# Kernel optimization log

Measured on AMD Instinct MI355X. Metric: run time of the kernel, lower is better.

The kernel has to match this reference:

```python
import jax, jax.numpy as jnp
import numpy as np

DT = 0.001
HIDDEN = 512
OUT = 128

def setup_inputs() -> dict:
    key = jax.random.key(0)
    k1, k2 = jax.random.split(key)
    x = jax.random.normal(k1, (64, 2048, HIDDEN), dtype=jnp.float32)
    # torch Linear default init ~ U(-1/sqrt(fan_in), 1/sqrt(fan_in)), weight shape [out, in]
    lim = 1.0 / np.sqrt(HIDDEN)
    W = jax.random.uniform(k2, (OUT, HIDDEN), dtype=jnp.float32, minval=-lim, maxval=lim)
    tau_syn = jnp.asarray(0.5, dtype=jnp.float32)  # tau_syn_out (used as tau_syn_inv)
    tau_mem = jnp.asarray(0.5, dtype=jnp.float32)  # tau_mem_out (used as tau_mem_inv)
    return {"x": x, "W": W, "tau_syn": tau_syn, "tau_mem": tau_mem}

def reference(x, W, tau_syn, tau_mem):
    # SNNDecode.forward: clamp taus, permute to [seq, batch, in], per-step
    # Linear + norse LI (leaky integrator) feed-forward step with v_leak = 0.
    tau_syn = jnp.clip(tau_syn, 0.0, 1.0)
    tau_mem = jnp.clip(tau_mem, 0.0, 1.0)
    batch, seq, _ = x.shape
    # The per-step Linear is recurrence-independent: hoist it into one big GEMM.
    # z_all: [seq, batch, out]
    z_all = jnp.einsum('bsh,oh->sbo', x, W)
    v0 = jnp.zeros((batch, OUT), dtype=x.dtype)
    i0 = jnp.zeros((batch, OUT), dtype=x.dtype)

    def step(carry, z):
        v, i = carry
        # li_feed_forward_step: dv = dt*tau_mem_inv*((v_leak - v) + i)
        v_new = v + DT * tau_mem * (i - v)
        i_dec = i - DT * tau_syn * i
        i_new = i_dec + z
        return (v_new, i_new), v_new

    (v_f, i_f), voltages = jax.lax.scan(step, (v0, i0), z_all)
    # output stacked over time: [seq, batch, out]; final state (v, i)
    return voltages, v_f, i_f
```

## Files before the change

### kernel.cpp

```cpp
#include <hip/hip_runtime.h>
#include <hip/hip_bf16.h>


typedef __attribute__((ext_vector_type(4))) float          f4;
typedef __attribute__((ext_vector_type(8))) short          s8;
typedef __attribute__((ext_vector_type(4))) unsigned       u4;
typedef __attribute__((ext_vector_type(2))) unsigned       u2;
typedef __attribute__((ext_vector_type(4))) unsigned short su4;

#define SEQ    2048
#define HID    512
#define CHAINS 8192
#define VOLT   16777216
#define NCH    64
#define CHUNK  32

__device__ __forceinline__ float clamp01(float x) { return fminf(fmaxf(x, 0.f), 1.f); }

__device__ __forceinline__ unsigned pkbf(float x, float y) {
  float2 t; t.x = x; t.y = y;
  union { __hip_bfloat162 h; unsigned u; } c;
  c.h = __float22bfloat162_rn(t);
  return c.u;
}

__device__ __forceinline__ unsigned short f2bf(float f) {
  union { float f; unsigned u; } c; c.f = f;
  unsigned u = c.u;
  unsigned r = (u + 0x7fffu + ((u >> 16) & 1u)) >> 16;
  return (unsigned short)r;
}

__device__ __forceinline__ float bf2f(unsigned short s) {
  union { unsigned u; float f; } c; c.u = ((unsigned)s) << 16; return c.f;
}

__device__ __forceinline__ int swz(int row, int k) {
  return (row * 64 + k) ^ ((row & 7) << 3);
}

__global__ __launch_bounds__(256) void k_wconv(const float* __restrict__ W,
                                               unsigned short* __restrict__ Wb) {
  const int i = blockIdx.x * 256 + threadIdx.x;
  const f4 lo = ((const f4*)W)[2 * i];
  const f4 hi = ((const f4*)W)[2 * i + 1];
  su4 v0, v1;
#pragma unroll
  for (int j = 0; j < 4; ++j) { v0[j] = f2bf(lo[j]); v1[j] = f2bf(hi[j]); }
  ((su4*)Wb)[2 * i] = v0;
  ((su4*)Wb)[2 * i + 1] = v1;
}

template <int ZB>
__global__ __launch_bounds__(256, 2) void k_gemm(const float* __restrict__ X,
                                                 const unsigned short* __restrict__ Wb,
                                                 float* __restrict__ Out,
                                                 unsigned short* __restrict__ zbf,
                                                 const float* __restrict__ tau_syn,
                                                 const float* __restrict__ tau_mem,
                                                 float* __restrict__ ws) {
  __shared__ __align__(16) char smem[65536];
  short* const AS = (short*)smem;
  float* const ZS = (float*)smem;

  const int tid = threadIdx.x;
  const int blk = blockIdx.x;
  const int m0  = blk << 7;
  const int bI  = blk >> 4;
  const int t0  = (blk & 15) << 7;

  const int rbase = tid >> 3;
  const int coff  = (tid & 7) << 3;

  const int lane = tid & 63;
  const int wid  = tid >> 6;
  const int wmb  = (wid >> 1) << 6;
  const int wnb  = (wid & 1) << 6;
  const int lr   = lane & 15;
  const int lk   = (lane >> 4) << 3;

  const float* pX[4];
#pragma unroll
  for (int c = 0; c < 4; ++c)
    pX[c] = X + (size_t)(m0 + (c << 5) + rbase) * HID + coff;
  const unsigned short* pB[4];
#pragma unroll
  for (int ni = 0; ni < 4; ++ni)
    pB[ni] = Wb + (size_t)(wnb + (ni << 4) + lr) * HID + lk;

  f4 acc[4][4];
#pragma unroll
  for (int mi = 0; mi < 4; ++mi)
#pragma unroll
    for (int ni = 0; ni < 4; ++ni) acc[mi][ni] = (f4){0.f, 0.f, 0.f, 0.f};

  f4 xa[3][4][2];
#pragma unroll
  for (int c = 0; c < 4; ++c) {
    xa[0][c][0] = *(const f4*)(pX[c]);
    xa[0][c][1] = *(const f4*)(pX[c] + 4);
    xa[1][c][0] = *(const f4*)(pX[c] + 64);
    xa[1][c][1] = *(const f4*)(pX[c] + 68);
  }

#pragma unroll
  for (int ks = 0; ks < 8; ++ks) {
    const int cur = ks % 3;
    short* const Ac = AS + ((ks & 1) << 13);
#pragma unroll
    for (int c = 0; c < 4; ++c) {
      const int row = (c << 5) + rbase;
      u4 va;
      va[0] = pkbf(xa[cur][c][0][0], xa[cur][c][0][1]);
      va[1] = pkbf(xa[cur][c][0][2], xa[cur][c][0][3]);
      va[2] = pkbf(xa[cur][c][1][0], xa[cur][c][1][1]);
      va[3] = pkbf(xa[cur][c][1][2], xa[cur][c][1][3]);
      *(u4*)&Ac[swz(row, coff)] = va;
    }
    __syncthreads();
    s8 bg[2][4];
#pragma unroll
    for (int kk = 0; kk < 2; ++kk)
#pragma unroll
      for (int ni = 0; ni < 4; ++ni)
        bg[kk][ni] = *(const s8*)(pB[ni] + (ks << 6) + (kk << 5));
    if (ks < 6) {
      const int k0 = (ks + 2) << 6;
      const int nxt = (ks + 2) % 3;
#pragma unroll
      for (int c = 0; c < 4; ++c) {
        xa[nxt][c][0] = *(const f4*)(pX[c] + k0);
        xa[nxt][c][1] = *(const f4*)(pX[c] + k0 + 4);
      }
    }
#pragma unroll
    for (int kk = 0; kk < 2; ++kk) {
      s8 af[4];
#pragma unroll
      for (int mi = 0; mi < 4; ++mi)
        af[mi] = *(const s8*)&Ac[swz(wmb + (mi << 4) + lr, (kk << 5) + lk)];
#pragma unroll
      for (int mi = 0; mi < 4; ++mi)
#pragma unroll
        for (int ni = 0; ni < 4; ++ni)
          acc[mi][ni] = __builtin_amdgcn_mfma_f32_16x16x32_bf16(af[mi], bg[kk][ni],
                                                                acc[mi][ni], 0, 0, 0);
    }
  }

  __syncthreads();
  const int rr = (lane >> 4) << 2;
#pragma unroll
  for (int mi = 0; mi < 4; ++mi)
#pragma unroll
    for (int ni = 0; ni < 4; ++ni)
#pragma unroll
      for (int r = 0; r < 4; ++r)
        ZS[(wmb + (mi << 4) + rr + r) * 128 + wnb + (ni << 4) + lr] = acc[mi][ni][r];
  __syncthreads();

  if (ZB) {
    unsigned short* const Zrow = zbf + (size_t)t0 * 8192 + (bI << 7);
#pragma unroll
    for (int i = 0; i < 16; ++i) {
      const int idx  = (i << 8) + tid;
      const int toff = idx >> 5;
      const int c4   = idx & 31;
      const f4 zv = *(const f4*)&ZS[toff * 128 + (c4 << 2)];
      u2 pk; pk[0] = pkbf(zv[0], zv[1]); pk[1] = pkbf(zv[2], zv[3]);
      *(u2*)(Zrow + (size_t)toff * 8192 + (c4 << 2)) = pk;
    }
  } else {
    float* const Zrow = Out + (size_t)t0 * 8192 + (bI << 7);
#pragma unroll
    for (int i = 0; i < 16; ++i) {
      const int idx  = (i << 8) + tid;
      const int toff = idx >> 5;
      const int c4   = idx & 31;
      *(f4*)(Zrow + (size_t)toff * 8192 + (c4 << 2)) = *(const f4*)&ZS[toff * 128 + (c4 << 2)];
    }
  }
  {
    const float a  = 0.001f * clamp01(tau_mem[0]);
    const float eb = 1.f - 0.001f * clamp01(tau_syn[0]);
    const int col = tid & 127, h = tid >> 7;
    const int chain = (bI << 7) + col;
#pragma unroll
    for (int s = 0; s < 2; ++s) {
      const int r0 = (h << 6) + (s << 5);
      const float* zs = ZS + r0 * 128 + col;
      float v = 0.f, ii = 0.f;
#pragma unroll 8
      for (int j = 0; j < CHUNK; ++j) {
        const float z = zs[j * 128];
        v  = v + a * (ii - v);
        ii = eb * ii + z;
      }
      const int q = ((blk & 15) << 2) + (h << 1) + s;
      ws[q * CHAINS + chain]                 = v;
      ws[NCH * CHAINS + q * CHAINS + chain]  = ii;
    }
  }
}

__global__ __launch_bounds__(256) void k_comb(const float* __restrict__ tau_syn,
                                              const float* __restrict__ tau_mem,
                                              float* __restrict__ Out,
                                              float* __restrict__ ws) {
  __shared__ __align__(16) f4 SV[NCH][4], SI[NCH][4];
  const int tid = threadIdx.x;
  const int q   = tid >> 2;
  const int s   = tid & 3;
  const int cg  = blockIdx.x * 4 + s;
  const float a  = 0.001f * clamp01(tau_mem[0]);
  const float bb = 0.001f * clamp01(tau_syn[0]);
  const float ea = 1.f - a, eb = 1.f - bb;
  float P = 1.f, Q = 0.f, R = 1.f;
#pragma unroll
  for (int j = 0; j < CHUNK; ++j) { const float Pn = P * ea; Q = P * a + Q * eb; P = Pn; R *= eb; }

  f4* vend = (f4*)ws;
  f4* iend = vend + NCH * 2048;
  f4 xv = vend[q * 2048 + cg];
  f4 xi = iend[q * 2048 + cg];
  SV[q][s] = xv; SI[q][s] = xi;

  float Pd = P, Qd = Q, Rd = R;
#pragma unroll
  for (int d = 1; d < NCH; d <<= 1) {
    __syncthreads();
    f4 av, ai;
    const bool val = (q >= d);
    if (val) { av = SV[q - d][s]; ai = SI[q - d][s]; }
    __syncthreads();
    if (val) {
      xv = xv + Pd * av + Qd * ai;
      xi = xi + Rd * ai;
      SV[q][s] = xv; SI[q][s] = xi;
    }
    const float Pn = Pd * Pd;
    Qd = Pd * Qd + Qd * Rd;
    Pd = Pn;
    Rd = Rd * Rd;
  }
  __syncthreads();
  f4 iv = (f4){0.f, 0.f, 0.f, 0.f}, ij = (f4){0.f, 0.f, 0.f, 0.f};
  if (q > 0) { iv = SV[q - 1][s]; ij = SI[q - 1][s]; }
  vend[q * 2048 + cg] = iv;
  iend[q * 2048 + cg] = ij;
  if (q == NCH - 1) {
    ((f4*)(Out + VOLT))[cg]          = xv;
    ((f4*)(Out + VOLT + CHAINS))[cg] = xi;
  }
}

template <int ZB>
__global__ __launch_bounds__(256) void k_emit(const float* __restrict__ tau_syn,
                                              const float* __restrict__ tau_mem,
                                              float* __restrict__ Out,
                                              const unsigned short* __restrict__ zbf,
                                              const float* __restrict__ ws) {
  const int tid = threadIdx.x;
  const int cg = (blockIdx.x & 31) * 64 + (tid & 63);
  const int q  = (blockIdx.x >> 5) * 4 + (tid >> 6);
  const float a  = 0.001f * clamp01(tau_mem[0]);
  const float eb = 1.f - 0.001f * clamp01(tau_syn[0]);

  const f4* vin = (const f4*)ws;
  const f4* iin = vin + NCH * 2048;
  f4 v  = vin[q * 2048 + cg];
  f4 ii = iin[q * 2048 + cg];

  f4* o4 = (f4*)Out;
  const int tb = q << 5;
#pragma unroll 8
  for (int j = 0; j < CHUNK; ++j) {
    const size_t idx = (size_t)(tb + j) * 2048 + cg;
    f4 z;
    if (ZB) {
      const su4 zb = *(const su4*)(zbf + (((size_t)(tb + j)) << 13) + (cg << 2));
      z[0] = bf2f(zb[0]); z[1] = bf2f(zb[1]); z[2] = bf2f(zb[2]); z[3] = bf2f(zb[3]);
    } else {
      z = o4[idx];
    }
    v  = v + a * (ii - v);
    o4[idx] = v;
    ii = eb * ii + z;
  }
}

extern "C" void kernel_launch(void* const* d_in, const int* in_sizes, int n_in,
                              void* d_out, int out_size, void* d_ws, size_t ws_size,
                              hipStream_t stream) {
  const float* X   = (const float*)d_in[0];
  const float* W   = (const float*)d_in[1];
  const float* tsy = (const float*)d_in[2];
  const float* tme = (const float*)d_in[3];
  float* Out = (float*)d_out;
  float* ws  = (float*)d_ws;
  unsigned short* Wb  = (unsigned short*)((char*)d_ws + (4u << 20));
  unsigned short* zbf = (unsigned short*)((char*)d_ws + (4u << 20) + (128u << 10));
  const size_t need = (4ull << 20) + (128ull << 10) + (32ull << 20);

  k_wconv<<<32, 256, 0, stream>>>(W, Wb);
  if (ws_size >= need) {
    k_gemm<1><<<1024, 256, 0, stream>>>(X, Wb, Out, zbf, tsy, tme, ws);
    k_comb<<<512, 256, 0, stream>>>(tsy, tme, Out, ws);
    k_emit<1><<<512, 256, 0, stream>>>(tsy, tme, Out, zbf, ws);
  } else {
    k_gemm<0><<<1024, 256, 0, stream>>>(X, Wb, Out, zbf, tsy, tme, ws);
    k_comb<<<512, 256, 0, stream>>>(tsy, tme, Out, ws);
    k_emit<0><<<512, 256, 0, stream>>>(tsy, tme, Out, zbf, ws);
  }
}
```

Before: 105.0 us.

## Load GEMM A fragments directly from global, drop LDS staging, bf16 Z tile

The GEMM no longer stages X through shared memory. Each wave loads its own 32-row A fragments straight from global memory into registers, converts them to bf16, and feeds them to MFMA, with the full 128-column W operand double-buffered in registers. The output tile is staged in LDS as bf16 with an XOR swizzle, which halves LDS use from 64KB to 32KB and removes the per-k-step barriers. The trade-offs are more register pressure from 16 accumulators plus 16 B fragments, possibly less coalesced X loads, and the chunk scan now reading z values rounded to bf16.

```diff
diff --git a/kernel.cpp b/kernel.cpp
--- a/kernel.cpp
+++ b/kernel.cpp
@@ -35,8 +35,8 @@
   union { unsigned u; float f; } c; c.u = ((unsigned)s) << 16; return c.f;
 }
 
-__device__ __forceinline__ int swz(int row, int k) {
-  return (row * 64 + k) ^ ((row & 7) << 3);
+__device__ __forceinline__ int zidx(int row, int col) {
+  return row * 128 + (col ^ (((row >> 2) & 7) << 4));
 }
 
 __global__ __launch_bounds__(256) void k_wconv(const float* __restrict__ W,
@@ -59,9 +59,7 @@
                                                  const float* __restrict__ tau_syn,
                                                  const float* __restrict__ tau_mem,
                                                  float* __restrict__ ws) {
-  __shared__ __align__(16) char smem[65536];
-  short* const AS = (short*)smem;
-  float* const ZS = (float*)smem;
+  __shared__ __align__(16) unsigned short ZSb[128 * 128];
 
   const int tid = threadIdx.x;
   const int blk = blockIdx.x;
@@ -69,115 +67,99 @@
   const int bI  = blk >> 4;
   const int t0  = (blk & 15) << 7;
 
-  const int rbase = tid >> 3;
-  const int coff  = (tid & 7) << 3;
-
   const int lane = tid & 63;
-  const int wid  = tid >> 6;
-  const int wmb  = (wid >> 1) << 6;
-  const int wnb  = (wid & 1) << 6;
+  const int w    = tid >> 6;
   const int lr   = lane & 15;
   const int lk   = (lane >> 4) << 3;
 
-  const float* pX[4];
-#pragma unroll
-  for (int c = 0; c < 4; ++c)
-    pX[c] = X + (size_t)(m0 + (c << 5) + rbase) * HID + coff;
-  const unsigned short* pB[4];
-#pragma unroll
-  for (int ni = 0; ni < 4; ++ni)
-    pB[ni] = Wb + (size_t)(wnb + (ni << 4) + lr) * HID + lk;
-
-  f4 acc[4][4];
-#pragma unroll
-  for (int mi = 0; mi < 4; ++mi)
-#pragma unroll
-    for (int ni = 0; ni < 4; ++ni) acc[mi][ni] = (f4){0.f, 0.f, 0.f, 0.f};
-
-  f4 xa[3][4][2];
-#pragma unroll
-  for (int c = 0; c < 4; ++c) {
-    xa[0][c][0] = *(const f4*)(pX[c]);
-    xa[0][c][1] = *(const f4*)(pX[c] + 4);
-    xa[1][c][0] = *(const f4*)(pX[c] + 64);
-    xa[1][c][1] = *(const f4*)(pX[c] + 68);
-  }
-
-#pragma unroll
-  for (int ks = 0; ks < 8; ++ks) {
-    const int cur = ks % 3;
-    short* const Ac = AS + ((ks & 1) << 13);
-#pragma unroll
-    for (int c = 0; c < 4; ++c) {
-      const int row = (c << 5) + rbase;
-      u4 va;
-      va[0] = pkbf(xa[cur][c][0][0], xa[cur][c][0][1]);
-      va[1] = pkbf(xa[cur][c][0][2], xa[cur][c][0][3]);
-      va[2] = pkbf(xa[cur][c][1][0], xa[cur][c][1][1]);
-      va[3] = pkbf(xa[cur][c][1][2], xa[cur][c][1][3]);
-      *(u4*)&Ac[swz(row, coff)] = va;
-    }
-    __syncthreads();
-    s8 bg[2][4];
-#pragma unroll
-    for (int kk = 0; kk < 2; ++kk)
-#pragma unroll
-      for (int ni = 0; ni < 4; ++ni)
-        bg[kk][ni] = *(const s8*)(pB[ni] + (ks << 6) + (kk << 5));
-    if (ks < 6) {
-      const int k0 = (ks + 2) << 6;
-      const int nxt = (ks + 2) % 3;
-#pragma unroll
-      for (int c = 0; c < 4; ++c) {
-        xa[nxt][c][0] = *(const f4*)(pX[c] + k0);
-        xa[nxt][c][1] = *(const f4*)(pX[c] + k0 + 4);
+  const float* pa[2];
+#pragma unroll
+  for (int mi = 0; mi < 2; ++mi)
+    pa[mi] = X + (size_t)(m0 + (w << 5) + (mi << 4) + lr) * HID + lk;
+  const unsigned short* pb[8];
+#pragma unroll
+  for (int ni = 0; ni < 8; ++ni)
+    pb[ni] = Wb + (size_t)((ni << 4) + lr) * HID + lk;
+
+  f4 acc[2][8];
+#pragma unroll
+  for (int mi = 0; mi < 2; ++mi)
+#pragma unroll
+    for (int ni = 0; ni < 8; ++ni) acc[mi][ni] = (f4){0.f, 0.f, 0.f, 0.f};
+
+  f4 xa[3][2][2];
+  s8 bg[2][8];
+#pragma unroll
+  for (int mi = 0; mi < 2; ++mi) {
+    xa[0][mi][0] = *(const f4*)(pa[mi]);
+    xa[0][mi][1] = *(const f4*)(pa[mi] + 4);
+  }
+#pragma unroll
+  for (int ni = 0; ni < 8; ++ni) bg[0][ni] = *(const s8*)(pb[ni]);
+#pragma unroll
+  for (int mi = 0; mi < 2; ++mi) {
+    xa[1][mi][0] = *(const f4*)(pa[mi] + 32);
+    xa[1][mi][1] = *(const f4*)(pa[mi] + 36);
+  }
+
+#pragma unroll
+  for (int k = 0; k < 16; ++k) {
+    const int cur = k % 3, kb = k & 1;
+    if (k < 15) {
+#pragma unroll
+      for (int ni = 0; ni < 8; ++ni)
+        bg[kb ^ 1][ni] = *(const s8*)(pb[ni] + ((k + 1) << 5));
+    }
+    if (k < 14) {
+      const int nxt = (k + 2) % 3;
+#pragma unroll
+      for (int mi = 0; mi < 2; ++mi) {
+        xa[nxt][mi][0] = *(const f4*)(pa[mi] + ((k + 2) << 5));
+        xa[nxt][mi][1] = *(const f4*)(pa[mi] + ((k + 2) << 5) + 4);
       }
     }
-#pragma unroll
-    for (int kk = 0; kk < 2; ++kk) {
-      s8 af[4];
-#pragma unroll
-      for (int mi = 0; mi < 4; ++mi)
-        af[mi] = *(const s8*)&Ac[swz(wmb + (mi << 4) + lr, (kk << 5) + lk)];
-#pragma unroll
-      for (int mi = 0; mi < 4; ++mi)
-#pragma unroll
-        for (int ni = 0; ni < 4; ++ni)
-          acc[mi][ni] = __builtin_amdgcn_mfma_f32_16x16x32_bf16(af[mi], bg[kk][ni],
-                                                                acc[mi][ni], 0, 0, 0);
-    }
-  }
-
+    s8 af[2];
+#pragma unroll
+    for (int mi = 0; mi < 2; ++mi) {
+      union { u4 u; s8 s; } t;
+      t.u[0] = pkbf(xa[cur][mi][0][0], xa[cur][mi][0][1]);
+      t.u[1] = pkbf(xa[cur][mi][0][2], xa[cur][mi][0][3]);
+      t.u[2] = pkbf(xa[cur][mi][1][0], xa[cur][mi][1][1]);
+      t.u[3] = pkbf(xa[cur][mi][1][2], xa[cur][mi][1][3]);
+      af[mi] = t.s;
+    }
+#pragma unroll
+    for (int mi = 0; mi < 2; ++mi)
+#pragma unroll
+      for (int ni = 0; ni < 8; ++ni)
+        acc[mi][ni] = __builtin_amdgcn_mfma_f32_16x16x32_bf16(af[mi], bg[kb][ni],
+                                                              acc[mi][ni], 0, 0, 0);
+  }
+
+  const int rr = (lane >> 4) << 2;
+#pragma unroll
+  for (int mi = 0; mi < 2; ++mi)
+#pragma unroll
+    for (int ni = 0; ni < 8; ++ni)
+#pragma unroll
+      for (int r = 0; r < 4; ++r)
+        ZSb[zidx((w << 5) + (mi << 4) + rr + r, (ni << 4) + lr)] =
+            f2bf(acc[mi][ni][r]);
   __syncthreads();
-  const int rr = (lane >> 4) << 2;
-#pragma unroll
-  for (int mi = 0; mi < 4; ++mi)
-#pragma unroll
-    for (int ni = 0; ni < 4; ++ni)
-#pragma unroll
-      for (int r = 0; r < 4; ++r)
-        ZS[(wmb + (mi << 4) + rr + r) * 128 + wnb + (ni << 4) + lr] = acc[mi][ni][r];
-  __syncthreads();
-
-  if (ZB) {
-    unsigned short* const Zrow = zbf + (size_t)t0 * 8192 + (bI << 7);
-#pragma unroll
-    for (int i = 0; i < 16; ++i) {
-      const int idx  = (i << 8) + tid;
-      const int toff = idx >> 5;
-      const int c4   = idx & 31;
-      const f4 zv = *(const f4*)&ZS[toff * 128 + (c4 << 2)];
-      u2 pk; pk[0] = pkbf(zv[0], zv[1]); pk[1] = pkbf(zv[2], zv[3]);
-      *(u2*)(Zrow + (size_t)toff * 8192 + (c4 << 2)) = pk;
-    }
-  } else {
-    float* const Zrow = Out + (size_t)t0 * 8192 + (bI << 7);
-#pragma unroll
-    for (int i = 0; i < 16; ++i) {
-      const int idx  = (i << 8) + tid;
-      const int toff = idx >> 5;
-      const int c4   = idx & 31;
-      *(f4*)(Zrow + (size_t)toff * 8192 + (c4 << 2)) = *(const f4*)&ZS[toff * 128 + (c4 << 2)];
+
+#pragma unroll
+  for (int i = 0; i < 16; ++i) {
+    const int idx  = (i << 8) + tid;
+    const int toff = idx >> 5;
+    const int c4   = idx & 31;
+    const int colp = (c4 << 2) ^ (((toff >> 2) & 7) << 4);
+    const su4 zb = *(const su4*)&ZSb[toff * 128 + colp];
+    if (ZB) {
+      *(su4*)(zbf + (size_t)(t0 + toff) * 8192 + (bI << 7) + (c4 << 2)) = zb;
+    } else {
+      f4 zf; zf[0] = bf2f(zb[0]); zf[1] = bf2f(zb[1]);
+      zf[2] = bf2f(zb[2]); zf[3] = bf2f(zb[3]);
+      *(f4*)(Out + (size_t)(t0 + toff) * 8192 + (bI << 7) + (c4 << 2)) = zf;
     }
   }
   {
@@ -188,11 +170,10 @@
 #pragma unroll
     for (int s = 0; s < 2; ++s) {
       const int r0 = (h << 6) + (s << 5);
-      const float* zs = ZS + r0 * 128 + col;
       float v = 0.f, ii = 0.f;
 #pragma unroll 8
       for (int j = 0; j < CHUNK; ++j) {
-        const float z = zs[j * 128];
+        const float z = bf2f(ZSb[zidx(r0 + j, col)]);
         v  = v + a * (ii - v);
         ii = eb * ii + z;
       }
```

After: 160.2 us. +52.5%, slower.
